# Kernel tuning notes

Measured on AMD Instinct MI355X. Metric: run time of the kernel, lower is better.

## Reference

```python
import jax, jax.numpy as jnp
import numpy as np

EPS = 1e-12

def _l2norm(x):
    # F.normalize(p=2, dim=1) with eps clamp on the norm
    n = jnp.linalg.norm(x, axis=1, keepdims=True)
    return x / jnp.maximum(n, EPS)

def _xavier_uniform(key, shape, gain=1.414):
    fan_in, fan_out = shape[-1], shape[0]
    a = gain * np.sqrt(6.0 / (fan_in + fan_out))
    return jax.random.uniform(key, shape, jnp.float32, -a, a)

def setup_inputs() -> dict:
    NUM_ENT, NUM_REL, D, E, B = 100000, 500, 512, 150000, 4096
    key = jax.random.key(0)
    ks = jax.random.split(key, 12)
    heads = jax.random.randint(ks[0], (B, 1), 0, NUM_ENT)
    rels  = jax.random.randint(ks[1], (B, 1), 0, NUM_REL)
    tails = jax.random.randint(ks[2], (B, 1), 0, NUM_ENT)
    triples = jnp.concatenate([heads, rels, tails], axis=1)           # [B,3]
    node_list = jax.random.randint(ks[3], (2, E), 0, NUM_ENT)          # [2,E] (src,dst)
    edge_list = jax.random.randint(ks[4], (E,), 0, NUM_REL)            # [E] relation per edge
    return {
        "triples": triples,
        "node_list": node_list,
        "edge_list": edge_list,
        "ent_emb_init": jax.random.normal(ks[5], (NUM_ENT, D), jnp.float32),
        "rel_emb_init": jax.random.normal(ks[6], (NUM_REL, D), jnp.float32),
        "W_1": _xavier_uniform(ks[7], (D, D)),
        "W_a": _xavier_uniform(ks[8], (1, D)),
        "g_0": _xavier_uniform(ks[9], (1, D)),
        "W_E": _xavier_uniform(ks[10], (D, D)),
        "W_R": _xavier_uniform(ks[11], (D, D)),
    }

def reference(triples, node_list, edge_list, ent_emb_init, rel_emb_init,
              W_1, W_a, g_0, W_E, W_R):
    num_ent = ent_emb_init.shape[0]
    e0 = _l2norm(ent_emb_init)                      # normalized entity table [N,D]
    src, dst = node_list[0], node_list[1]
    h_i = e0[src]                                   # [E,D]
    h_j = e0[dst]                                   # [E,D]
    g_k = rel_emb_init[edge_list]                   # [E,D]

    # c_ijk = W_1 @ (h_j*g_k)^T  -> kept edge-major as [E,D]
    c = (h_j * g_k) @ W_1.T                         # [E,D]
    a = -jax.nn.leaky_relu((h_i * jnp.tanh(c)) @ W_a[0], 0.2)   # [E]
    c_base = (h_i * g_0) @ W_1.T                    # [E,D]
    a_base = -jax.nn.leaky_relu((h_i * jnp.tanh(c_base)) @ W_a[0], 0.2)  # [E]

    a_exp = jnp.exp(a)                              # [E]
    ab_exp = jnp.exp(a_base)                        # [E]

    # segment-softmax denominator: sum of edge exps per source node + baseline term
    a_exp_sum = jax.ops.segment_sum(a_exp[:, None], src, num_segments=num_ent)  # [N,1]
    # baseline exp depends only on src node -> duplicate scatter-set writes identical values
    ab_sorted = jnp.zeros_like(a_exp_sum).at[src].set(ab_exp[:, None])           # [N,1]
    denom = ab_sorted + a_exp_sum
    denom = jnp.where(denom == 0.0, EPS, denom)

    # weighted scatter-aggregate of messages (dropout omitted: eval-mode identity)
    ac = a_exp[:, None] * c                         # [E,D]
    ac_base = ab_exp[:, None] * c_base              # [E,D]
    a_new = jax.ops.segment_sum(ac, src, num_segments=num_ent)                   # [N,D]
    ab_new = jnp.zeros_like(a_new).at[src].set(ac_base)                          # [N,D]

    h_prime = jax.nn.elu((ab_new + a_new) / denom)  # [N,D]
    ent_new = _l2norm(e0 @ W_E + h_prime)           # [N,D]
    rel_new = rel_emb_init @ W_R                    # [R,D]

    head = ent_new[triples[:, 0]][:, None, :]       # [B,1,D]
    rel  = rel_new[triples[:, 1]][:, None, :]       # [B,1,D]
    tail = ent_new[triples[:, 2]][:, None, :]       # [B,1,D]
    return jnp.concatenate([head, rel, tail], axis=1)  # [B,3,D]
```

## Files before the change

### kernel.cpp

```cpp
#include <hip/hip_runtime.h>
#include <cmath>


#define DDIM 512
#define MAXM 65536
#define BM 64
#define BN 64
#define BK 32
#define LSTR 40

typedef __attribute__((ext_vector_type(8))) short short8;
typedef __attribute__((ext_vector_type(4))) float fv4;

__device__ __forceinline__ float elu1(float x) { return x > 0.f ? x : expm1f(x); }
__device__ __forceinline__ float sexp(float x) {
    float lr = x >= 0.f ? x : 0.2f * x;
    return expf(-lr);
}
__device__ __forceinline__ unsigned short f2bf(float x) {
    unsigned u = __float_as_uint(x);
    u += 0x7FFFu + ((u >> 16) & 1u);
    return (unsigned short)(u >> 16);
}
__device__ __forceinline__ float bf2f(unsigned short h) {
    return __uint_as_float((unsigned)h << 16);
}

__global__ __launch_bounds__(128)
void invnorm_sel_kernel(const float* __restrict__ emb, const int* __restrict__ slotNode,
                        const int* __restrict__ rowsL, const int* __restrict__ dstIdx,
                        const int* __restrict__ Mdev, int NS, float* __restrict__ invN)
{
    __shared__ float ws2[2];
    int total = NS + min(MAXM, *Mdev);
    int t = threadIdx.x;
    for (int q = blockIdx.x; q < total; q += gridDim.x) {
        int n = (q < NS) ? slotNode[q] : dstIdx[rowsL[q - NS]];
        float4 v = *(const float4*)(emb + (size_t)n * DDIM + t * 4);
        float s = v.x*v.x + v.y*v.y + v.z*v.z + v.w*v.w;
        #pragma unroll
        for (int off = 32; off > 0; off >>= 1) s += __shfl_down(s, off);
        if ((t & 63) == 0) ws2[t >> 6] = s;
        __syncthreads();
        if (t == 0) invN[n] = 1.f / fmaxf(sqrtf(ws2[0] + ws2[1]), 1e-12f);
        __syncthreads();
    }
}

__global__ __launch_bounds__(128)
void l2norm_kernel(float* __restrict__ data)
{
    int r = blockIdx.x, t = threadIdx.x;
    size_t o = (size_t)r * DDIM + t * 4;
    float4 v = *(const float4*)(data + o);
    float s = v.x*v.x + v.y*v.y + v.z*v.z + v.w*v.w;
    #pragma unroll
    for (int off = 32; off > 0; off >>= 1) s += __shfl_down(s, off);
    __shared__ float ws2[2];
    if ((t & 63) == 0) ws2[t >> 6] = s;
    __syncthreads();
    float inv = 1.f / fmaxf(sqrtf(ws2[0] + ws2[1]), 1e-12f);
    *(float4*)(data + o) = make_float4(v.x*inv, v.y*inv, v.z*inv, v.w*inv);
}

__global__ __launch_bounds__(256)
void transpose512_kernel(const float* __restrict__ in, float* __restrict__ out)
{
    __shared__ float tile[32][33];
    int bx = blockIdx.x & 15, by = blockIdx.x >> 4;
    int x = threadIdx.x & 31, y0 = (threadIdx.x >> 5) * 4;
    #pragma unroll
    for (int i = 0; i < 4; i++)
        tile[y0 + i][x] = in[(size_t)(by * 32 + y0 + i) * 512 + bx * 32 + x];
    __syncthreads();
    #pragma unroll
    for (int i = 0; i < 4; i++)
        out[(size_t)(bx * 32 + y0 + i) * 512 + by * 32 + x] = tile[x][y0 + i];
}

__global__ void hist_kernel(const int* __restrict__ src, int* __restrict__ cnt, int E)
{
    int e = blockIdx.x * 256 + threadIdx.x;
    if (e < E) atomicAdd(&cnt[src[e]], 1);
}

__global__ __launch_bounds__(1024)
void scan1_kernel(const int* __restrict__ in, int* __restrict__ out,
                  int* __restrict__ blockTot, int n)
{
    __shared__ int sh[1024];
    int t = threadIdx.x;
    int i = blockIdx.x * 1024 + t;
    int v = (i < n) ? in[i] : 0;
    sh[t] = v;
    __syncthreads();
    for (int off = 1; off < 1024; off <<= 1) {
        int x = (t >= off) ? sh[t - off] : 0;
        __syncthreads();
        sh[t] += x;
        __syncthreads();
    }
    if (i < n) out[i] = sh[t] - v;
    if (t == 1023) blockTot[blockIdx.x] = sh[1023];
}

__global__ __launch_bounds__(1024)
void scan2_kernel(const int* __restrict__ blockTot, int* __restrict__ blockOff,
                  int* __restrict__ outLast, int G)
{
    __shared__ int sh[1024];
    int t = threadIdx.x;
    int v = (t < G) ? blockTot[t] : 0;
    sh[t] = v;
    __syncthreads();
    for (int off = 1; off < 1024; off <<= 1) {
        int x = (t >= off) ? sh[t - off] : 0;
        __syncthreads();
        sh[t] += x;
        __syncthreads();
    }
    if (t < G) blockOff[t] = sh[t] - v;
    if (t == 1023) *outLast = sh[1023];
}

__global__ __launch_bounds__(1024)
void scan3_kernel(int* __restrict__ out, const int* __restrict__ blockOff, int n)
{
    int i = blockIdx.x * 1024 + threadIdx.x;
    if (i < n) out[i] += blockOff[blockIdx.x];
}

__global__ void bucket_kernel(const int* __restrict__ src, int* __restrict__ cursor,
                              int* __restrict__ edge_ids, int E)
{
    int e = blockIdx.x * 256 + threadIdx.x;
    if (e < E) { int p = atomicAdd(&cursor[src[e]], 1); edge_ids[p] = e; }
}

__global__ void slotnode_kernel(const int* __restrict__ triples,
                                int* __restrict__ slotNode, int NS)
{
    int r = blockIdx.x * 256 + threadIdx.x;
    if (r < NS) { int b = r >> 1, p = (r & 1) * 2; slotNode[r] = triples[b * 3 + p]; }
}

__global__ void deg_kernel(const int* __restrict__ slotNode, const int* __restrict__ rowSt,
                           int* __restrict__ deg, int NS)
{
    int r = blockIdx.x * 256 + threadIdx.x;
    if (r < NS) { int n = slotNode[r]; deg[r] = rowSt[n + 1] - rowSt[n]; }
}

__global__ void fill_rows_kernel(const int* __restrict__ slotNode, const int* __restrict__ rowSt,
                                 const int* __restrict__ edgeIds, const int* __restrict__ slotOff,
                                 int* __restrict__ rows, int NS)
{
    int r = blockIdx.x * 256 + threadIdx.x;
    if (r >= NS) return;
    int n = slotNode[r];
    int gs = rowSt[n], d = rowSt[n + 1] - gs, mo = slotOff[r];
    for (int j = 0; j < d && mo + j < MAXM; j++) rows[mo + j] = edgeIds[gs + j];
}

template<int AMODE, int EPI, bool DEVM>
__global__ __launch_bounds__(256)
void gemm_mfma_k(const float* __restrict__ entEmb, const float* __restrict__ invNorm,
                 const int* __restrict__ rowsList, const int* __restrict__ srcIdx,
                 const int* __restrict__ dstIdx,  const int* __restrict__ relIdx,
                 const float* __restrict__ relEmb, const float* __restrict__ g0,
                 const int* __restrict__ slotNode, const float* __restrict__ Adense,
                 const float* __restrict__ Bmat,   const float* __restrict__ Wa,
                 float* __restrict__ scoreOut,     const float* __restrict__ invDenom,
                 const float* __restrict__ Hadd,   float* __restrict__ Cout,
                 int Mhost, const int* __restrict__ Mdev)
{
    __shared__ unsigned short AsH[BM][LSTR], AsL[BM][LSTR];
    __shared__ unsigned short BsH[BN][LSTR], BsL[BN][LSTR];

    int M = DEVM ? min(MAXM, *Mdev) : Mhost;
    int tid  = threadIdx.x;
    int lane = tid & 63, wid = tid >> 6;
    int waveM = wid >> 1, waveN = wid & 1;
    int quad = lane >> 4, l15 = lane & 15;
    int n0 = blockIdx.y * BN;

    int sRow = tid >> 2;
    int sSeg = (tid & 3) * 8;

    for (int mt = blockIdx.x; mt * BM < M; mt += gridDim.x) {
        int m0 = mt * BM;
        int amc = min(m0 + sRow, M - 1);
        const float* aP = nullptr; const float* aP2 = nullptr;
        float aScale = 1.f;
        if (AMODE == 0) {
            int e = rowsList[amc];
            int dn = dstIdx[e], rn = relIdx[e];
            aP  = entEmb + (size_t)dn * DDIM + sSeg;
            aP2 = relEmb + (size_t)rn * DDIM + sSeg;
            aScale = invNorm[dn];
        } else if (AMODE == 1) {
            int n = slotNode[amc];
            aP  = entEmb + (size_t)n * DDIM + sSeg;
            aP2 = g0 + sSeg;
            aScale = invNorm[n];
        } else if (AMODE == 2) {
            aP = Adense + (size_t)amc * DDIM + sSeg;
        } else {
            int n = slotNode[amc];
            aP = entEmb + (size_t)n * DDIM + sSeg;
            aScale = invNorm[n];
        }
        const float* bP = Bmat + (size_t)(n0 + sRow) * DDIM + sSeg;

        fv4 acc[2][2];
        #pragma unroll
        for (int i = 0; i < 2; i++)
            #pragma unroll
            for (int j = 0; j < 2; j++) acc[i][j] = fv4{0.f, 0.f, 0.f, 0.f};

        for (int kt = 0; kt < DDIM; kt += BK) {
            __syncthreads();
            {
                float va[8];
                float4 x0 = *(const float4*)(aP + kt);
                float4 x1 = *(const float4*)(aP + kt + 4);
                va[0]=x0.x; va[1]=x0.y; va[2]=x0.z; va[3]=x0.w;
                va[4]=x1.x; va[5]=x1.y; va[6]=x1.z; va[7]=x1.w;
                if (AMODE == 0 || AMODE == 1) {
                    float4 y0 = *(const float4*)(aP2 + kt);
                    float4 y1 = *(const float4*)(aP2 + kt + 4);
                    va[0]*=y0.x; va[1]*=y0.y; va[2]*=y0.z; va[3]*=y0.w;
                    va[4]*=y1.x; va[5]*=y1.y; va[6]*=y1.z; va[7]*=y1.w;
                }
                short8 h8, l8;
                #pragma unroll
                for (int i = 0; i < 8; i++) {
                    float x = va[i] * aScale;
                    unsigned short h = f2bf(x);
                    h8[i] = (short)h;
                    l8[i] = (short)f2bf(x - bf2f(h));
                }
                *(short8*)&AsH[sRow][sSeg] = h8;
                *(short8*)&AsL[sRow][sSeg] = l8;
            }
            {
                float4 x0 = *(const float4*)(bP + kt);
                float4 x1 = *(const float4*)(bP + kt + 4);
                float vb[8] = {x0.x,x0.y,x0.z,x0.w,x1.x,x1.y,x1.z,x1.w};
                short8 h8, l8;
                #pragma unroll
                for (int i = 0; i < 8; i++) {
                    unsigned short h = f2bf(vb[i]);
                    h8[i] = (short)h;
                    l8[i] = (short)f2bf(vb[i] - bf2f(h));
                }
                *(short8*)&BsH[sRow][sSeg] = h8;
                *(short8*)&BsL[sRow][sSeg] = l8;
            }
            __syncthreads();

            short8 aH[2], aL[2], bH[2], bL[2];
            #pragma unroll
            for (int i = 0; i < 2; i++) {
                int ar = waveM * 32 + i * 16 + l15;
                aH[i] = *(const short8*)&AsH[ar][quad * 8];
                aL[i] = *(const short8*)&AsL[ar][quad * 8];
                int br = waveN * 32 + i * 16 + l15;
                bH[i] = *(const short8*)&BsH[br][quad * 8];
                bL[i] = *(const short8*)&BsL[br][quad * 8];
            }
            #pragma unroll
            for (int i = 0; i < 2; i++)
                #pragma unroll
                for (int j = 0; j < 2; j++) {
                    acc[i][j] = __builtin_amdgcn_mfma_f32_16x16x32_bf16(aH[i], bH[j], acc[i][j], 0, 0, 0);
                    acc[i][j] = __builtin_amdgcn_mfma_f32_16x16x32_bf16(aH[i], bL[j], acc[i][j], 0, 0, 0);
                    acc[i][j] = __builtin_amdgcn_mfma_f32_16x16x32_bf16(aL[i], bH[j], acc[i][j], 0, 0, 0);
                }
        }

        if (EPI == 1) {
            #pragma unroll
            for (int i = 0; i < 2; i++) {
                #pragma unroll
                for (int reg = 0; reg < 4; reg++) {
                    int gm = m0 + waveM * 32 + i * 16 + quad * 4 + reg;
                    bool valid = gm < M;
                    int gmc = valid ? gm : 0;
                    int srcn = (AMODE == 0) ? srcIdx[rowsList[gmc]] : slotNode[gmc];
                    float invs = invNorm[srcn];
                    float s = 0.f;
                    #pragma unroll
                    for (int j = 0; j < 2; j++) {
                        int col = n0 + waveN * 32 + j * 16 + l15;
                        float hv = entEmb[(size_t)srcn * DDIM + col];
                        float wv = Wa[col];
                        s += tanhf(acc[i][j][reg]) * hv * wv;
                    }
                    s *= invs;
                    s += __shfl_xor(s, 8); s += __shfl_xor(s, 4);
                    s += __shfl_xor(s, 2); s += __shfl_xor(s, 1);
                    if (l15 == 0 && valid) atomicAdd(scoreOut + gm, s);
                }
            }
        } else {
            #pragma unroll
            for (int i = 0; i < 2; i++) {
                #pragma unroll
                for (int reg = 0; reg < 4; reg++) {
                    int gm = m0 + waveM * 32 + i * 16 + quad * 4 + reg;
                    if (gm >= M) continue;
                    #pragma unroll
                    for (int j = 0; j < 2; j++) {
                        int col = n0 + waveN * 32 + j * 16 + l15;
                        size_t o = (size_t)gm * DDIM + col;
                        float v = acc[i][j][reg];
                        if (EPI == 2) v = elu1(v * invDenom[gm]);
                        else if (EPI == 3) v += Hadd[o];
                        Cout[o] = v;
                    }
                }
            }
        }
    }
}

__global__ __launch_bounds__(128)
void build_p_kernel(const float* __restrict__ entEmb, const float* __restrict__ invNorm,
                    const float* __restrict__ relEmb, const float* __restrict__ g0,
                    const int* __restrict__ slotNode, const int* __restrict__ rowSt,
                    const int* __restrict__ edgeIds, const int* __restrict__ dstIdx,
                    const int* __restrict__ relIdx, const int* __restrict__ slotOff,
                    const float* __restrict__ scoreE, const float* __restrict__ scoreS,
                    float* __restrict__ P, float* __restrict__ invDenom)
{
    int r = blockIdx.x, t = threadIdx.x;
    int n = slotNode[r];
    int gs = rowSt[n], d = rowSt[n + 1] - gs;
    size_t po = (size_t)r * DDIM + t * 4;
    if (d == 0) {
        *(float4*)(P + po) = make_float4(0.f, 0.f, 0.f, 0.f);
        if (t == 0) invDenom[r] = 1.f;
        return;
    }
    int mo = slotOff[r];
    float ab = sexp(scoreS[r]);
    float sc = ab * invNorm[n];
    float4 ev = *(const float4*)(entEmb + (size_t)n * DDIM + t * 4);
    float4 gv = *(const float4*)(g0 + t * 4);
    float4 acc = make_float4(sc*ev.x*gv.x, sc*ev.y*gv.y, sc*ev.z*gv.z, sc*ev.w*gv.w);
    float denom = ab;
    for (int j = 0; j < d; j++) {
        if (mo + j >= MAXM) break;
        int e = edgeIds[gs + j];
        float ae = sexp(scoreE[mo + j]);
        int dn = dstIdx[e], rl = relIdx[e];
        float s = ae * invNorm[dn];
        float4 dv = *(const float4*)(entEmb + (size_t)dn * DDIM + t * 4);
        float4 rv = *(const float4*)(relEmb + (size_t)rl * DDIM + t * 4);
        acc.x = fmaf(s, dv.x*rv.x, acc.x);
        acc.y = fmaf(s, dv.y*rv.y, acc.y);
        acc.z = fmaf(s, dv.z*rv.z, acc.z);
        acc.w = fmaf(s, dv.w*rv.w, acc.w);
        denom += ae;
    }
    *(float4*)(P + po) = acc;
    if (t == 0) invDenom[r] = 1.f / denom;
}

__global__ __launch_bounds__(128)
void gather_out_kernel(const int* __restrict__ triples, const float* __restrict__ ENT,
                       const float* __restrict__ relnew, float* __restrict__ out)
{
    int r = blockIdx.x;
    int b = r / 3, j = r - b * 3;
    const float* srow;
    if (j == 1) srow = relnew + (size_t)triples[r] * DDIM;
    else        srow = ENT + (size_t)(b * 2 + (j == 2 ? 1 : 0)) * DDIM;
    int t = threadIdx.x * 4;
    *(float4*)(out + (size_t)r * DDIM + t) = *(const float4*)(srow + t);
}

extern "C" void kernel_launch(void* const* d_in, const int* in_sizes, int n_in,
                              void* d_out, int out_size, void* d_ws, size_t ws_size,
                              hipStream_t stream)
{
    const int*   triples = (const int*)  d_in[0];
    const int*   nodes   = (const int*)  d_in[1];
    const int*   edges   = (const int*)  d_in[2];
    const float* entEmb  = (const float*)d_in[3];
    const float* relEmb  = (const float*)d_in[4];
    const float* W1      = (const float*)d_in[5];
    const float* Wa      = (const float*)d_in[6];
    const float* g0      = (const float*)d_in[7];
    const float* WE      = (const float*)d_in[8];
    const float* WR      = (const float*)d_in[9];

    const int B  = in_sizes[0] / 3;
    const int E  = in_sizes[2];
    const int N  = in_sizes[3] / DDIM;
    const int R  = in_sizes[4] / DDIM;
    const int NS = 2 * B;
    const int* srcIdx = nodes;
    const int* dstIdx = nodes + E;

    char* ws = (char*)d_ws;
    size_t off = 0;
    auto carve = [&](size_t bytes) -> void* {
        void* p = ws + off;
        off = (off + bytes + 255) & ~(size_t)255;
        return p;
    };
    float* P        = (float*)carve((size_t)NS * DDIM * 4);
    float* H        = (float*)carve((size_t)NS * DDIM * 4);
    float* ENT      = (float*)carve((size_t)NS * DDIM * 4);
    float* relnew   = (float*)carve((size_t)R * DDIM * 4);
    float* WET      = (float*)carve((size_t)DDIM * DDIM * 4);
    float* WRT      = (float*)carve((size_t)DDIM * DDIM * 4);
    float* invNorm  = (float*)carve((size_t)N * 4);
    float* score_e  = (float*)carve((size_t)MAXM * 4);
    float* score_s  = (float*)carve((size_t)NS * 4);
    float* invDen   = (float*)carve((size_t)NS * 4);
    int*   cnt      = (int*)carve((size_t)N * 4);
    int*   rowSt    = (int*)carve((size_t)(N + 1) * 4);
    int*   cursor   = (int*)carve((size_t)N * 4);
    int*   edgeIds  = (int*)carve((size_t)E * 4);
    int*   slotNode = (int*)carve((size_t)NS * 4);
    int*   deg      = (int*)carve((size_t)NS * 4);
    int*   slotOff  = (int*)carve((size_t)(NS + 1) * 4);
    int*   rowsL    = (int*)carve((size_t)MAXM * 4);
    int*   blockTot = (int*)carve((size_t)1024 * 4);
    int*   blockOff = (int*)carve((size_t)1024 * 4);
    (void)ws_size; (void)n_in; (void)out_size;

    auto scan = [&](const int* in, int* out, int n) {
        int G = (n + 1023) / 1024;
        scan1_kernel<<<G, 1024, 0, stream>>>(in, out, blockTot, n);
        scan2_kernel<<<1, 1024, 0, stream>>>(blockTot, blockOff, out + n, G);
        scan3_kernel<<<G, 1024, 0, stream>>>(out, blockOff, n);
    };

    hipMemsetAsync(cnt, 0, (size_t)N * 4, stream);
    hist_kernel<<<(E + 255) / 256, 256, 0, stream>>>(srcIdx, cnt, E);
    scan(cnt, rowSt, N);
    hipMemcpyAsync(cursor, rowSt, (size_t)N * 4, hipMemcpyDeviceToDevice, stream);
    bucket_kernel<<<(E + 255) / 256, 256, 0, stream>>>(srcIdx, cursor, edgeIds, E);

    slotnode_kernel<<<(NS + 255) / 256, 256, 0, stream>>>(triples, slotNode, NS);
    deg_kernel<<<(NS + 255) / 256, 256, 0, stream>>>(slotNode, rowSt, deg, NS);
    scan(deg, slotOff, NS);
    fill_rows_kernel<<<(NS + 255) / 256, 256, 0, stream>>>(slotNode, rowSt, edgeIds,
                                                           slotOff, rowsL, NS);
    const int* Mdev = slotOff + NS;

    invnorm_sel_kernel<<<4096, 128, 0, stream>>>(entEmb, slotNode, rowsL, dstIdx,
                                                 Mdev, NS, invNorm);

    transpose512_kernel<<<256, 256, 0, stream>>>(WE, WET);
    transpose512_kernel<<<256, 256, 0, stream>>>(WR, WRT);

    hipMemsetAsync(score_e, 0, (size_t)MAXM * 4, stream);
    hipMemsetAsync(score_s, 0, (size_t)NS * 4, stream);
    dim3 gEdge(256, DDIM / BN);
    gemm_mfma_k<0, 1, true><<<gEdge, 256, 0, stream>>>(
        entEmb, invNorm, rowsL, srcIdx, dstIdx, edges, relEmb, g0, slotNode,
        nullptr, W1, Wa, score_e, nullptr, nullptr, nullptr, 0, Mdev);
    dim3 gSlot((NS + BM - 1) / BM, DDIM / BN);
    gemm_mfma_k<1, 1, false><<<gSlot, 256, 0, stream>>>(
        entEmb, invNorm, nullptr, nullptr, nullptr, nullptr, relEmb, g0, slotNode,
        nullptr, W1, Wa, score_s, nullptr, nullptr, nullptr, NS, nullptr);

    build_p_kernel<<<NS, 128, 0, stream>>>(entEmb, invNorm, relEmb, g0, slotNode,
                                           rowSt, edgeIds, dstIdx, edges, slotOff,
                                           score_e, score_s, P, invDen);

    gemm_mfma_k<2, 2, false><<<gSlot, 256, 0, stream>>>(
        entEmb, invNorm, nullptr, nullptr, nullptr, nullptr, relEmb, g0, slotNode,
        P, W1, nullptr, nullptr, invDen, nullptr, H, NS, nullptr);

    gemm_mfma_k<3, 3, false><<<gSlot, 256, 0, stream>>>(
        entEmb, invNorm, nullptr, nullptr, nullptr, nullptr, relEmb, g0, slotNode,
        nullptr, WET, nullptr, nullptr, nullptr, H, ENT, NS, nullptr);
    l2norm_kernel<<<NS, 128, 0, stream>>>(ENT);

    dim3 gRel((R + BM - 1) / BM, DDIM / BN);
    gemm_mfma_k<2, 0, false><<<gRel, 256, 0, stream>>>(
        entEmb, invNorm, nullptr, nullptr, nullptr, nullptr, relEmb, g0, slotNode,
        relEmb, WRT, nullptr, nullptr, nullptr, nullptr, relnew, R, nullptr);

    gather_out_kernel<<<B * 3, 128, 0, stream>>>(triples, ENT, relnew, (float*)d_out);
}
```

Measured before the change: 516.6 us.

## Pre-split operands into MFMA fragment layout and use register-streamed 128x128 GEMM

Adds pre-pass kernels that gather, scale and split A and B operands into bf16 hi/lo arrays stored in MFMA fragment order. The GEMM kernel then streams fragments straight from global memory into registers with one-step prefetch, with no LDS staging or barriers. Tiles grow to 128x128 with 4x4 accumulators per wave. The aim is to stop redoing the fp32-to-bf16 split inside every GEMM tile and to raise MFMA density. The cost is extra kernels, large workspace buffers and more global traffic for the fragment arrays.

Result: slower. 592.0 us (+14.6%).

```diff
diff --git a/kernel.cpp b/kernel.cpp
--- a/kernel.cpp
+++ b/kernel.cpp
@@ -4,26 +4,33 @@
 
 #define DDIM 512
 #define MAXM 65536
-#define BM 64
-#define BN 64
-#define BK 32
-#define LSTR 40
+#define GBM 128
+#define GBN 128
 
 typedef __attribute__((ext_vector_type(8))) short short8;
 typedef __attribute__((ext_vector_type(4))) float fv4;
+typedef unsigned short u16;
 
 __device__ __forceinline__ float elu1(float x) { return x > 0.f ? x : expm1f(x); }
 __device__ __forceinline__ float sexp(float x) {
     float lr = x >= 0.f ? x : 0.2f * x;
     return expf(-lr);
 }
-__device__ __forceinline__ unsigned short f2bf(float x) {
+__device__ __forceinline__ u16 f2bf(float x) {
     unsigned u = __float_as_uint(x);
     u += 0x7FFFu + ((u >> 16) & 1u);
-    return (unsigned short)(u >> 16);
-}
-__device__ __forceinline__ float bf2f(unsigned short h) {
+    return (u16)(u >> 16);
+}
+__device__ __forceinline__ float bf2f(u16 h) {
     return __uint_as_float((unsigned)h << 16);
+}
+__device__ __forceinline__ void cvt8(const float* v, short8& h8, short8& l8) {
+    #pragma unroll
+    for (int i = 0; i < 8; i++) {
+        u16 h = f2bf(v[i]);
+        h8[i] = (short)h;
+        l8[i] = (short)f2bf(v[i] - bf2f(h));
+    }
 }
 
 __global__ __launch_bounds__(128)
@@ -137,162 +144,213 @@
     if (e < E) { int p = atomicAdd(&cursor[src[e]], 1); edge_ids[p] = e; }
 }
 
-__global__ void slotnode_kernel(const int* __restrict__ triples,
-                                int* __restrict__ slotNode, int NS)
+__global__ void slotdeg_kernel(const int* __restrict__ triples, const int* __restrict__ rowSt,
+                               int* __restrict__ slotNode, int* __restrict__ deg, int NS)
 {
     int r = blockIdx.x * 256 + threadIdx.x;
-    if (r < NS) { int b = r >> 1, p = (r & 1) * 2; slotNode[r] = triples[b * 3 + p]; }
-}
-
-__global__ void deg_kernel(const int* __restrict__ slotNode, const int* __restrict__ rowSt,
-                           int* __restrict__ deg, int NS)
-{
-    int r = blockIdx.x * 256 + threadIdx.x;
-    if (r < NS) { int n = slotNode[r]; deg[r] = rowSt[n + 1] - rowSt[n]; }
+    if (r < NS) {
+        int b = r >> 1, p = (r & 1) * 2;
+        int n = triples[b * 3 + p];
+        slotNode[r] = n;
+        deg[r] = rowSt[n + 1] - rowSt[n];
+    }
 }
 
 __global__ void fill_rows_kernel(const int* __restrict__ slotNode, const int* __restrict__ rowSt,
                                  const int* __restrict__ edgeIds, const int* __restrict__ slotOff,
-                                 int* __restrict__ rows, int NS)
+                                 int* __restrict__ rows, int* __restrict__ srcL, int NS)
 {
     int r = blockIdx.x * 256 + threadIdx.x;
     if (r >= NS) return;
     int n = slotNode[r];
     int gs = rowSt[n], d = rowSt[n + 1] - gs, mo = slotOff[r];
-    for (int j = 0; j < d && mo + j < MAXM; j++) rows[mo + j] = edgeIds[gs + j];
-}
-
-template<int AMODE, int EPI, bool DEVM>
+    for (int j = 0; j < d && mo + j < MAXM; j++) {
+        rows[mo + j] = edgeIds[gs + j];
+        srcL[mo + j] = n;
+    }
+}
+
 __global__ __launch_bounds__(256)
-void gemm_mfma_k(const float* __restrict__ entEmb, const float* __restrict__ invNorm,
-                 const int* __restrict__ rowsList, const int* __restrict__ srcIdx,
-                 const int* __restrict__ dstIdx,  const int* __restrict__ relIdx,
-                 const float* __restrict__ relEmb, const float* __restrict__ g0,
-                 const int* __restrict__ slotNode, const float* __restrict__ Adense,
-                 const float* __restrict__ Bmat,   const float* __restrict__ Wa,
-                 float* __restrict__ scoreOut,     const float* __restrict__ invDenom,
-                 const float* __restrict__ Hadd,   float* __restrict__ Cout,
+void afrag_dense_kernel(const float* __restrict__ in, int rows,
+                        u16* __restrict__ hi, u16* __restrict__ lo)
+{
+    int nt = ((rows + 127) >> 7) << 3;
+    int wid = threadIdx.x >> 6, lane = threadIdx.x & 63;
+    int l15 = lane & 15, seg = (lane >> 4) * 8;
+    for (int rt = blockIdx.x * 4 + wid; rt < nt; rt += gridDim.x * 4) {
+        int r = min(rt * 16 + l15, rows - 1);
+        const float* p = in + (size_t)r * DDIM + seg;
+        size_t base = (size_t)rt * 8192 + (size_t)lane * 8;
+        #pragma unroll 4
+        for (int kt = 0; kt < 16; kt++) {
+            float4 x0 = *(const float4*)(p + kt * 32);
+            float4 x1 = *(const float4*)(p + kt * 32 + 4);
+            float v[8] = {x0.x, x0.y, x0.z, x0.w, x1.x, x1.y, x1.z, x1.w};
+            short8 h8, l8; cvt8(v, h8, l8);
+            *(short8*)(hi + base + (size_t)kt * 512) = h8;
+            *(short8*)(lo + base + (size_t)kt * 512) = l8;
+        }
+    }
+}
+
+__global__ __launch_bounds__(256)
+void afrag_edge_kernel(const float* __restrict__ entEmb, const float* __restrict__ invN,
+                       const float* __restrict__ relEmb, const int* __restrict__ rowsL,
+                       const int* __restrict__ dstIdx, const int* __restrict__ relIdx,
+                       const int* __restrict__ Mdev,
+                       u16* __restrict__ hi, u16* __restrict__ lo)
+{
+    int M = max(1, min(MAXM, *Mdev));
+    int nt = ((M + 127) >> 7) << 3;
+    int wid = threadIdx.x >> 6, lane = threadIdx.x & 63;
+    int l15 = lane & 15, seg = (lane >> 4) * 8;
+    for (int rt = blockIdx.x * 4 + wid; rt < nt; rt += gridDim.x * 4) {
+        int m = min(rt * 16 + l15, M - 1);
+        int e = rowsL[m];
+        int dn = dstIdx[e], rl = relIdx[e];
+        float sc = invN[dn];
+        const float* ep = entEmb + (size_t)dn * DDIM + seg;
+        const float* rp = relEmb + (size_t)rl * DDIM + seg;
+        size_t base = (size_t)rt * 8192 + (size_t)lane * 8;
+        #pragma unroll 4
+        for (int kt = 0; kt < 16; kt++) {
+            float4 x0 = *(const float4*)(ep + kt * 32);
+            float4 x1 = *(const float4*)(ep + kt * 32 + 4);
+            float4 y0 = *(const float4*)(rp + kt * 32);
+            float4 y1 = *(const float4*)(rp + kt * 32 + 4);
+            float v[8] = {sc*x0.x*y0.x, sc*x0.y*y0.y, sc*x0.z*y0.z, sc*x0.w*y0.w,
+                          sc*x1.x*y1.x, sc*x1.y*y1.y, sc*x1.z*y1.z, sc*x1.w*y1.w};
+            short8 h8, l8; cvt8(v, h8, l8);
+            *(short8*)(hi + base + (size_t)kt * 512) = h8;
+            *(short8*)(lo + base + (size_t)kt * 512) = l8;
+        }
+    }
+}
+
+__global__ __launch_bounds__(256)
+void afrag_slot_kernel(const float* __restrict__ entEmb, const float* __restrict__ invN,
+                       const float* __restrict__ g0, const int* __restrict__ slotNode,
+                       int NS, u16* __restrict__ s1h, u16* __restrict__ s1l,
+                       u16* __restrict__ s3h, u16* __restrict__ s3l)
+{
+    int nt = ((NS + 127) >> 7) << 3;
+    int wid = threadIdx.x >> 6, lane = threadIdx.x & 63;
+    int l15 = lane & 15, seg = (lane >> 4) * 8;
+    for (int rt = blockIdx.x * 4 + wid; rt < nt; rt += gridDim.x * 4) {
+        int r = min(rt * 16 + l15, NS - 1);
+        int n = slotNode[r];
+        float sc = invN[n];
+        const float* ep = entEmb + (size_t)n * DDIM + seg;
+        const float* gp = g0 + seg;
+        size_t base = (size_t)rt * 8192 + (size_t)lane * 8;
+        #pragma unroll 2
+        for (int kt = 0; kt < 16; kt++) {
+            float4 x0 = *(const float4*)(ep + kt * 32);
+            float4 x1 = *(const float4*)(ep + kt * 32 + 4);
+            float4 y0 = *(const float4*)(gp + kt * 32);
+            float4 y1 = *(const float4*)(gp + kt * 32 + 4);
+            float v3[8] = {sc*x0.x, sc*x0.y, sc*x0.z, sc*x0.w,
+                           sc*x1.x, sc*x1.y, sc*x1.z, sc*x1.w};
+            float v1[8] = {v3[0]*y0.x, v3[1]*y0.y, v3[2]*y0.z, v3[3]*y0.w,
+                           v3[4]*y1.x, v3[5]*y1.y, v3[6]*y1.z, v3[7]*y1.w};
+            short8 h8, l8;
+            cvt8(v3, h8, l8);
+            *(short8*)(s3h + base + (size_t)kt * 512) = h8;
+            *(short8*)(s3l + base + (size_t)kt * 512) = l8;
+            cvt8(v1, h8, l8);
+            *(short8*)(s1h + base + (size_t)kt * 512) = h8;
+            *(short8*)(s1l + base + (size_t)kt * 512) = l8;
+        }
+    }
+}
+
+template<int EPI, bool DEVM>
+__global__ __launch_bounds__(256)
+void gemm_frag_k(const u16* __restrict__ Ahi, const u16* __restrict__ Alo,
+                 const u16* __restrict__ Bhi, const u16* __restrict__ Blo,
+                 const float* __restrict__ entEmb, const float* __restrict__ invNorm,
+                 const int* __restrict__ srcMap, const float* __restrict__ Wa,
+                 float* __restrict__ scoreOut, const float* __restrict__ invDenom,
+                 const float* __restrict__ Hadd, float* __restrict__ Cout,
                  int Mhost, const int* __restrict__ Mdev)
 {
-    __shared__ unsigned short AsH[BM][LSTR], AsL[BM][LSTR];
-    __shared__ unsigned short BsH[BN][LSTR], BsL[BN][LSTR];
-
-    int M = DEVM ? min(MAXM, *Mdev) : Mhost;
-    int tid  = threadIdx.x;
-    int lane = tid & 63, wid = tid >> 6;
+    int M = DEVM ? max(1, min(MAXM, *Mdev)) : Mhost;
+    int lane = threadIdx.x & 63, wid = threadIdx.x >> 6;
     int waveM = wid >> 1, waveN = wid & 1;
     int quad = lane >> 4, l15 = lane & 15;
-    int n0 = blockIdx.y * BN;
-
-    int sRow = tid >> 2;
-    int sSeg = (tid & 3) * 8;
-
-    for (int mt = blockIdx.x; mt * BM < M; mt += gridDim.x) {
-        int m0 = mt * BM;
-        int amc = min(m0 + sRow, M - 1);
-        const float* aP = nullptr; const float* aP2 = nullptr;
-        float aScale = 1.f;
-        if (AMODE == 0) {
-            int e = rowsList[amc];
-            int dn = dstIdx[e], rn = relIdx[e];
-            aP  = entEmb + (size_t)dn * DDIM + sSeg;
-            aP2 = relEmb + (size_t)rn * DDIM + sSeg;
-            aScale = invNorm[dn];
-        } else if (AMODE == 1) {
-            int n = slotNode[amc];
-            aP  = entEmb + (size_t)n * DDIM + sSeg;
-            aP2 = g0 + sSeg;
-            aScale = invNorm[n];
-        } else if (AMODE == 2) {
-            aP = Adense + (size_t)amc * DDIM + sSeg;
-        } else {
-            int n = slotNode[amc];
-            aP = entEmb + (size_t)n * DDIM + sSeg;
-            aScale = invNorm[n];
-        }
-        const float* bP = Bmat + (size_t)(n0 + sRow) * DDIM + sSeg;
-
-        fv4 acc[2][2];
+    int n0 = blockIdx.y * GBN;
+
+    for (int mt = blockIdx.x; mt * GBM < M; mt += gridDim.x) {
+        int m0 = mt * GBM;
+        const u16 *aHp[4], *aLp[4], *bHp[4], *bLp[4];
         #pragma unroll
-        for (int i = 0; i < 2; i++)
+        for (int i = 0; i < 4; i++) {
+            size_t rt = (size_t)(m0 >> 4) + waveM * 4 + i;
+            aHp[i] = Ahi + rt * 8192 + (size_t)lane * 8;
+            aLp[i] = Alo + rt * 8192 + (size_t)lane * 8;
+            size_t ntb = (size_t)(n0 >> 4) + waveN * 4 + i;
+            bHp[i] = Bhi + ntb * 8192 + (size_t)lane * 8;
+            bLp[i] = Blo + ntb * 8192 + (size_t)lane * 8;
+        }
+
+        fv4 acc[4][4];
+        #pragma unroll
+        for (int i = 0; i < 4; i++)
             #pragma unroll
-            for (int j = 0; j < 2; j++) acc[i][j] = fv4{0.f, 0.f, 0.f, 0.f};
-
-        for (int kt = 0; kt < DDIM; kt += BK) {
-            __syncthreads();
-            {
-                float va[8];
-                float4 x0 = *(const float4*)(aP + kt);
-                float4 x1 = *(const float4*)(aP + kt + 4);
-                va[0]=x0.x; va[1]=x0.y; va[2]=x0.z; va[3]=x0.w;
-                va[4]=x1.x; va[5]=x1.y; va[6]=x1.z; va[7]=x1.w;
-                if (AMODE == 0 || AMODE == 1) {
-                    float4 y0 = *(const float4*)(aP2 + kt);
-                    float4 y1 = *(const float4*)(aP2 + kt + 4);
-                    va[0]*=y0.x; va[1]*=y0.y; va[2]*=y0.z; va[3]*=y0.w;
-                    va[4]*=y1.x; va[5]*=y1.y; va[6]*=y1.z; va[7]*=y1.w;
+            for (int j = 0; j < 4; j++) acc[i][j] = fv4{0.f, 0.f, 0.f, 0.f};
+
+        short8 aH[4], aL[4], bH[4], bL[4];
+        #pragma unroll
+        for (int i = 0; i < 4; i++) {
+            aH[i] = *(const short8*)aHp[i];
+            aL[i] = *(const short8*)aLp[i];
+            bH[i] = *(const short8*)bHp[i];
+            bL[i] = *(const short8*)bLp[i];
+        }
+
+        for (int kt = 0; kt < 16; kt++) {
+            short8 nAH[4], nAL[4], nBH[4], nBL[4];
+            if (kt < 15) {
+                size_t o = (size_t)(kt + 1) * 512;
+                #pragma unroll
+                for (int i = 0; i < 4; i++) {
+                    nAH[i] = *(const short8*)(aHp[i] + o);
+                    nAL[i] = *(const short8*)(aLp[i] + o);
+                    nBH[i] = *(const short8*)(bHp[i] + o);
+                    nBL[i] = *(const short8*)(bLp[i] + o);
                 }
-                short8 h8, l8;
-                #pragma unroll
-                for (int i = 0; i < 8; i++) {
-                    float x = va[i] * aScale;
-                    unsigned short h = f2bf(x);
-                    h8[i] = (short)h;
-                    l8[i] = (short)f2bf(x - bf2f(h));
-                }
-                *(short8*)&AsH[sRow][sSeg] = h8;
-                *(short8*)&AsL[sRow][sSeg] = l8;
-            }
-            {
-                float4 x0 = *(const float4*)(bP + kt);
-                float4 x1 = *(const float4*)(bP + kt + 4);
-                float vb[8] = {x0.x,x0.y,x0.z,x0.w,x1.x,x1.y,x1.z,x1.w};
-                short8 h8, l8;
-                #pragma unroll
-                for (int i = 0; i < 8; i++) {
-                    unsigned short h = f2bf(vb[i]);
-                    h8[i] = (short)h;
-                    l8[i] = (short)f2bf(vb[i] - bf2f(h));
-                }
-                *(short8*)&BsH[sRow][sSeg] = h8;
-                *(short8*)&BsL[sRow][sSeg] = l8;
-            }
-            __syncthreads();
-
-            short8 aH[2], aL[2], bH[2], bL[2];
-            #pragma unroll
-            for (int i = 0; i < 2; i++) {
-                int ar = waveM * 32 + i * 16 + l15;
-                aH[i] = *(const short8*)&AsH[ar][quad * 8];
-                aL[i] = *(const short8*)&AsL[ar][quad * 8];
-                int br = waveN * 32 + i * 16 + l15;
-                bH[i] = *(const short8*)&BsH[br][quad * 8];
-                bL[i] = *(const short8*)&BsL[br][quad * 8];
             }
             #pragma unroll
-            for (int i = 0; i < 2; i++)
+            for (int i = 0; i < 4; i++)
                 #pragma unroll
-                for (int j = 0; j < 2; j++) {
+                for (int j = 0; j < 4; j++) {
                     acc[i][j] = __builtin_amdgcn_mfma_f32_16x16x32_bf16(aH[i], bH[j], acc[i][j], 0, 0, 0);
                     acc[i][j] = __builtin_amdgcn_mfma_f32_16x16x32_bf16(aH[i], bL[j], acc[i][j], 0, 0, 0);
                     acc[i][j] = __builtin_amdgcn_mfma_f32_16x16x32_bf16(aL[i], bH[j], acc[i][j], 0, 0, 0);
                 }
+            if (kt < 15) {
+                #pragma unroll
+                for (int i = 0; i < 4; i++) {
+                    aH[i] = nAH[i]; aL[i] = nAL[i];
+                    bH[i] = nBH[i]; bL[i] = nBL[i];
+                }
+            }
         }
 
         if (EPI == 1) {
             #pragma unroll
-            for (int i = 0; i < 2; i++) {
+            for (int i = 0; i < 4; i++) {
                 #pragma unroll
                 for (int reg = 0; reg < 4; reg++) {
-                    int gm = m0 + waveM * 32 + i * 16 + quad * 4 + reg;
+                    int gm = m0 + waveM * 64 + i * 16 + quad * 4 + reg;
                     bool valid = gm < M;
                     int gmc = valid ? gm : 0;
-                    int srcn = (AMODE == 0) ? srcIdx[rowsList[gmc]] : slotNode[gmc];
+                    int srcn = srcMap[gmc];
                     float invs = invNorm[srcn];
                     float s = 0.f;
                     #pragma unroll
-                    for (int j = 0; j < 2; j++) {
-                        int col = n0 + waveN * 32 + j * 16 + l15;
+                    for (int j = 0; j < 4; j++) {
+                        int col = n0 + waveN * 64 + j * 16 + l15;
                         float hv = entEmb[(size_t)srcn * DDIM + col];
                         float wv = Wa[col];
                         s += tanhf(acc[i][j][reg]) * hv * wv;
@@ -305,17 +363,18 @@
             }
         } else {
             #pragma unroll
-            for (int i = 0; i < 2; i++) {
+            for (int i = 0; i < 4; i++) {
                 #pragma unroll
                 for (int reg = 0; reg < 4; reg++) {
-                    int gm = m0 + waveM * 32 + i * 16 + quad * 4 + reg;
+                    int gm = m0 + waveM * 64 + i * 16 + quad * 4 + reg;
                     if (gm >= M) continue;
+                    float idv = (EPI == 2) ? invDenom[gm] : 0.f;
                     #pragma unroll
-                    for (int j = 0; j < 2; j++) {
-                        int col = n0 + waveN * 32 + j * 16 + l15;
+                    for (int j = 0; j < 4; j++) {
+                        int col = n0 + waveN * 64 + j * 16 + l15;
                         size_t o = (size_t)gm * DDIM + col;
                         float v = acc[i][j][reg];
-                        if (EPI == 2) v = elu1(v * invDenom[gm]);
+                        if (EPI == 2) v = elu1(v * idv);
                         else if (EPI == 3) v += Hadd[o];
                         Cout[o] = v;
                     }
@@ -411,6 +470,8 @@
         off = (off + bytes + 255) & ~(size_t)255;
         return p;
     };
+    const int NS128 = ((NS + 127) / 128) * 128;
+    const int R128  = ((R + 127) / 128) * 128;
     float* P        = (float*)carve((size_t)NS * DDIM * 4);
     float* H        = (float*)carve((size_t)NS * DDIM * 4);
     float* ENT      = (float*)carve((size_t)NS * DDIM * 4);
@@ -429,8 +490,25 @@
     int*   deg      = (int*)carve((size_t)NS * 4);
     int*   slotOff  = (int*)carve((size_t)(NS + 1) * 4);
     int*   rowsL    = (int*)carve((size_t)MAXM * 4);
+    int*   srcL     = (int*)carve((size_t)MAXM * 4);
     int*   blockTot = (int*)carve((size_t)1024 * 4);
     int*   blockOff = (int*)carve((size_t)1024 * 4);
+    u16* AeH = (u16*)carve((size_t)MAXM * DDIM * 2);
+    u16* AeL = (u16*)carve((size_t)MAXM * DDIM * 2);
+    u16* As1H = (u16*)carve((size_t)NS128 * DDIM * 2);
+    u16* As1L = (u16*)carve((size_t)NS128 * DDIM * 2);
+    u16* As3H = (u16*)carve((size_t)NS128 * DDIM * 2);
+    u16* As3L = (u16*)carve((size_t)NS128 * DDIM * 2);
+    u16* ApH = (u16*)carve((size_t)NS128 * DDIM * 2);
+    u16* ApL = (u16*)carve((size_t)NS128 * DDIM * 2);
+    u16* ArH = (u16*)carve((size_t)R128 * DDIM * 2);
+    u16* ArL = (u16*)carve((size_t)R128 * DDIM * 2);
+    u16* W1H = (u16*)carve((size_t)DDIM * DDIM * 2);
+    u16* W1L = (u16*)carve((size_t)DDIM * DDIM * 2);
+    u16* WEH = (u16*)carve((size_t)DDIM * DDIM * 2);
+    u16* WEL = (u16*)carve((size_t)DDIM * DDIM * 2);
+    u16* WRH = (u16*)carve((size_t)DDIM * DDIM * 2);
+    u16* WRL = (u16*)carve((size_t)DDIM * DDIM * 2);
     (void)ws_size; (void)n_in; (void)out_size;
 
     auto scan = [&](const int* in, int* out, int n) {
@@ -446,11 +524,10 @@
     hipMemcpyAsync(cursor, rowSt, (size_t)N * 4, hipMemcpyDeviceToDevice, stream);
     bucket_kernel<<<(E + 255) / 256, 256, 0, stream>>>(srcIdx, cursor, edgeIds, E);
 
-    slotnode_kernel<<<(NS + 255) / 256, 256, 0, stream>>>(triples, slotNode, NS);
-    deg_kernel<<<(NS + 255) / 256, 256, 0, stream>>>(slotNode, rowSt, deg, NS);
+    slotdeg_kernel<<<(NS + 255) / 256, 256, 0, stream>>>(triples, rowSt, slotNode, deg, NS);
     scan(deg, slotOff, NS);
     fill_rows_kernel<<<(NS + 255) / 256, 256, 0, stream>>>(slotNode, rowSt, edgeIds,
-                                                           slotOff, rowsL, NS);
+                                                           slotOff, rowsL, srcL, NS);
     const int* Mdev = slotOff + NS;
 
     invnorm_sel_kernel<<<4096, 128, 0, stream>>>(entEmb, slotNode, rowsL, dstIdx,
@@ -458,35 +535,45 @@
 
     transpose512_kernel<<<256, 256, 0, stream>>>(WE, WET);
     transpose512_kernel<<<256, 256, 0, stream>>>(WR, WRT);
+    afrag_dense_kernel<<<8, 256, 0, stream>>>(W1, DDIM, W1H, W1L);
+    afrag_dense_kernel<<<8, 256, 0, stream>>>(WET, DDIM, WEH, WEL);
+    afrag_dense_kernel<<<8, 256, 0, stream>>>(WRT, DDIM, WRH, WRL);
+
+    afrag_edge_kernel<<<128, 256, 0, stream>>>(entEmb, invNorm, relEmb, rowsL,
+                                               dstIdx, edges, Mdev, AeH, AeL);
+    afrag_slot_kernel<<<128, 256, 0, stream>>>(entEmb, invNorm, g0, slotNode, NS,
+                                               As1H, As1L, As3H, As3L);
 
     hipMemsetAsync(score_e, 0, (size_t)MAXM * 4, stream);
     hipMemsetAsync(score_s, 0, (size_t)NS * 4, stream);
-    dim3 gEdge(256, DDIM / BN);
-    gemm_mfma_k<0, 1, true><<<gEdge, 256, 0, stream>>>(
-        entEmb, invNorm, rowsL, srcIdx, dstIdx, edges, relEmb, g0, slotNode,
-        nullptr, W1, Wa, score_e, nullptr, nullptr, nullptr, 0, Mdev);
-    dim3 gSlot((NS + BM - 1) / BM, DDIM / BN);
-    gemm_mfma_k<1, 1, false><<<gSlot, 256, 0, stream>>>(
-        entEmb, invNorm, nullptr, nullptr, nullptr, nullptr, relEmb, g0, slotNode,
-        nullptr, W1, Wa, score_s, nullptr, nullptr, nullptr, NS, nullptr);
+    dim3 gEdge(128, DDIM / GBN);
+    gemm_frag_k<1, true><<<gEdge, 256, 0, stream>>>(
+        AeH, AeL, W1H, W1L, entEmb, invNorm, srcL, Wa,
+        score_e, nullptr, nullptr, nullptr, 0, Mdev);
+    dim3 gSlot((NS + GBM - 1) / GBM, DDIM / GBN);
+    gemm_frag_k<1, false><<<gSlot, 256, 0, stream>>>(
+        As1H, As1L, W1H, W1L, entEmb, invNorm, slotNode, Wa,
+        score_s, nullptr, nullptr, nullptr, NS, nullptr);
 
     build_p_kernel<<<NS, 128, 0, stream>>>(entEmb, invNorm, relEmb, g0, slotNode,
                                            rowSt, edgeIds, dstIdx, edges, slotOff,
                                            score_e, score_s, P, invDen);
 
-    gemm_mfma_k<2, 2, false><<<gSlot, 256, 0, stream>>>(
-        entEmb, invNorm, nullptr, nullptr, nullptr, nullptr, relEmb, g0, slotNode,
-        P, W1, nullptr, nullptr, invDen, nullptr, H, NS, nullptr);
-
-    gemm_mfma_k<3, 3, false><<<gSlot, 256, 0, stream>>>(
-        entEmb, invNorm, nullptr, nullptr, nullptr, nullptr, relEmb, g0, slotNode,
-        nullptr, WET, nullptr, nullptr, nullptr, H, ENT, NS, nullptr);
+    afrag_dense_kernel<<<128, 256, 0, stream>>>(P, NS, ApH, ApL);
+    gemm_frag_k<2, false><<<gSlot, 256, 0, stream>>>(
+        ApH, ApL, W1H, W1L, entEmb, invNorm, nullptr, nullptr,
+        nullptr, invDen, nullptr, H, NS, nullptr);
+
+    gemm_frag_k<3, false><<<gSlot, 256, 0, stream>>>(
+        As3H, As3L, WEH, WEL, entEmb, invNorm, nullptr, nullptr,
+        nullptr, nullptr, H, ENT, NS, nullptr);
     l2norm_kernel<<<NS, 128, 0, stream>>>(ENT);
 
-    dim3 gRel((R + BM - 1) / BM, DDIM / BN);
-    gemm_mfma_k<2, 0, false><<<gRel, 256, 0, stream>>>(
-        entEmb, invNorm, nullptr, nullptr, nullptr, nullptr, relEmb, g0, slotNode,
-        relEmb, WRT, nullptr, nullptr, nullptr, nullptr, relnew, R, nullptr);
+    afrag_dense_kernel<<<8, 256, 0, stream>>>(relEmb, R, ArH, ArL);
+    dim3 gRel((R + GBM - 1) / GBM, DDIM / GBN);
+    gemm_frag_k<0, false><<<gRel, 256, 0, stream>>>(
+        ArH, ArL, WRH, WRL, entEmb, invNorm, nullptr, nullptr,
+        nullptr, nullptr, nullptr, relnew, R, nullptr);
 
     gather_out_kernel<<<B * 3, 128, 0, stream>>>(triples, ENT, relnew, (float*)d_out);
 }
```
